# Kernel tuning notes

Measured on AMD Instinct MI355X. Metric: run time of the kernel, lower is better.

Reference implementation:

```python
import jax, jax.numpy as jnp
import numpy as np

H, N, B, L = 256, 64, 4, 2048
LN_EPS = 1e-5


def setup_inputs() -> dict:
    key = jax.random.key(0)
    ks = jax.random.split(key, 10)
    u = jax.random.normal(ks[0], (B, L, H), dtype=jnp.float32)
    # Parameters (HiPPO-eig init replaced by equivalent-range random init; same forward math).
    log_neg_real = jnp.log(jax.random.uniform(ks[1], (N,), minval=0.01, maxval=2.0))
    imag = jax.random.normal(ks[2], (N,)) * 3.0
    B_re = jax.random.normal(ks[3], (H, N)) * 0.01
    B_im = jax.random.normal(ks[4], (H, N)) * 0.01
    C_re = jax.random.normal(ks[5], (H, N)) * 0.01
    C_im = jax.random.normal(ks[6], (H, N)) * 0.01
    D = jax.random.normal(ks[7], (H,)) * 0.01
    log_step = jax.random.uniform(ks[8], (H,), minval=-4.0, maxval=-1.0)
    ln_gamma = jnp.ones((H,), dtype=jnp.float32)
    ln_beta = jnp.zeros((H,), dtype=jnp.float32)
    return {"u": u, "log_neg_real": log_neg_real, "imag": imag,
            "B_re": B_re, "B_im": B_im, "C_re": C_re, "C_im": C_im,
            "D": D, "log_step": log_step, "ln_gamma": ln_gamma, "ln_beta": ln_beta}


def reference(u, log_neg_real, imag, B_re, B_im, C_re, C_im, D, log_step, ln_gamma, ln_beta):
    Bb, Ll, Hh = u.shape
    Lam_re = -jnp.exp(log_neg_real)                      # (N,)
    step = jnp.clip(jnp.exp(log_step), 1e-5, 1.0)        # (H,)
    s_re = step[:, None] * Lam_re[None, :]               # (H,N)
    s_im = step[:, None] * imag[None, :]                 # (H,N)
    Bb_re = B_re * step[:, None]
    Bb_im = B_im * step[:, None]
    CB_re = C_re * Bb_re - C_im * Bb_im                  # (H,N)
    CB_im = C_re * Bb_im + C_im * Bb_re                  # (H,N)
    l_idx = jnp.arange(Ll, dtype=u.dtype)                # (L,)
    ls_re = s_re[:, None, :] * l_idx[None, :, None]      # (H,L,N)
    ls_im = s_im[:, None, :] * l_idx[None, :, None]      # (H,L,N)
    mag = jnp.exp(ls_re)
    K = (jnp.einsum('hn,hln->hl', CB_re, mag * jnp.cos(ls_im))
         - jnp.einsum('hn,hln->hl', CB_im, mag * jnp.sin(ls_im)))  # (H,L)
    # FFT circular conv with zero padding to 2L -> linear conv
    uT = jnp.transpose(u, (0, 2, 1))                     # (B,H,L)
    n = 2 * Ll
    u_f = jnp.fft.rfft(uT, n=n)
    K_f = jnp.fft.rfft(K, n=n)
    y = jnp.fft.irfft(u_f * K_f[None], n=n)[..., :Ll]    # (B,H,L)
    y = y + uT * D[None, :, None]
    y = jnp.transpose(y, (0, 2, 1))                      # (B,L,H)
    y = jax.nn.gelu(y, approximate=False)                # torch nn.GELU default = exact
    # dropout: eval mode (identity)
    mean = jnp.mean(y, axis=-1, keepdims=True)
    var = jnp.var(y, axis=-1, keepdims=True)
    y = (y - mean) / jnp.sqrt(var + LN_EPS) * ln_gamma + ln_beta
    return y
```

## Files before the change

kernel.cpp:

```cpp
#include <hip/hip_runtime.h>
#include <hip/hip_bf16.h>
#include <math.h>

#define Hn 256
#define Nn 64
#define Bn 4
#define Ln 2048
#define NC 32

typedef __attribute__((ext_vector_type(8))) short short8;
typedef __attribute__((ext_vector_type(4))) float f32x4;

#define MFMA16 __builtin_amdgcn_mfma_f32_16x16x32_bf16

#define AF1_STRIDE 8192
#define AF2_STRIDE 12288

__device__ inline short bf16hi(float x) {
    union { __hip_bfloat16 b; unsigned short u; } cv;
    cv.b = __float2bfloat16(x);
    return (short)cv.u;
}
__device__ inline float bf16f(short s) {
    union { __hip_bfloat16 b; unsigned short u; } cv;
    cv.u = (unsigned short)s;
    return __bfloat162float(cv.b);
}

#define CSQ(r, i) { float _nr = (r)*(r) - (i)*(i); (i) = 2.f*(r)*(i); (r) = _nr; }

__global__ __launch_bounds__(256)
void k_pre(const float* __restrict__ u, float* __restrict__ uT,
           const float* __restrict__ lnr, const float* __restrict__ im,
           const float* __restrict__ Bre, const float* __restrict__ Bim,
           const float* __restrict__ Cre, const float* __restrict__ Cim,
           const float* __restrict__ lstep,
           short* __restrict__ AF1, short* __restrict__ AF2,
           float* __restrict__ apar)
{
    __shared__ float sh[2][64][66];
    __shared__ float cbrL[64];
    __shared__ float kb[128];
    int bid = blockIdx.x;
    int tid = threadIdx.x;

    if (bid < 512) {
        int b  = bid >> 7;
        int h0 = ((bid >> 5) & 3) << 6;
        int l0 = (bid & 31) << 6;
        int c4 = tid & 15, rr = tid >> 4;
        #pragma unroll
        for (int i = 0; i < 4; ++i) {
            int r = rr + (i << 4);
            float4 v = *(const float4*)&u[((size_t)b * Ln + l0 + r) * Hn + h0 + (c4 << 2)];
            sh[0][r][(c4 << 2) + 0] = v.x;
            sh[0][r][(c4 << 2) + 1] = v.y;
            sh[0][r][(c4 << 2) + 2] = v.z;
            sh[0][r][(c4 << 2) + 3] = v.w;
        }
        __syncthreads();
        #pragma unroll
        for (int i = 0; i < 4; ++i) {
            int hr = (tid >> 4) + (i << 4);
            int lc = tid & 15;
            float4 v;
            v.x = sh[0][(lc << 2) + 0][hr];
            v.y = sh[0][(lc << 2) + 1][hr];
            v.z = sh[0][(lc << 2) + 2][hr];
            v.w = sh[0][(lc << 2) + 3][hr];
            *(float4*)&uT[((size_t)b * Hn + h0 + hr) * Ln + l0 + (lc << 2)] = v;
        }
        return;
    }

    int h    = bid - 512;
    int lane = tid & 63;
    int wv   = tid >> 6;
    int kq   = lane >> 4;
    int l15  = lane & 15;
    int mrow = (wv << 4) + l15;

    float st  = fminf(fmaxf(expf(lstep[h]), 1e-5f), 1.0f);
    float lam = -expf(lnr[lane]);
    float er  = expf(st * lam);
    float smv = st * im[lane];
    float ar  = er * cosf(smv);
    float ai  = er * sinf(smv);
    float bre = Bre[h * Nn + lane] * st;
    float bim = Bim[h * Nn + lane] * st;
    float crr = Cre[h * Nn + lane];
    float cii = Cim[h * Nn + lane];
    float cbr = crr * bre - cii * bim;
    float cbi = crr * bim + cii * bre;

    float a16r = ar, a16i = ai;
    CSQ(a16r, a16i); CSQ(a16r, a16i); CSQ(a16r, a16i); CSQ(a16r, a16i);
    float a32r = a16r, a32i = a16i; CSQ(a32r, a32i);
    float a48r = a32r * a16r - a32i * a16i;
    float a48i = a32r * a16i + a32i * a16r;
    float a64r = a32r, a64i = a32i; CSQ(a64r, a64i);
    if (tid < 64) {
        apar[(h * Nn + lane) * 2]     = a64r;
        apar[(h * Nn + lane) * 2 + 1] = a64i;
    }

    float pr = 1.f, pi = 0.f;
    if (wv == 1) { pr = a16r; pi = a16i; }
    else if (wv == 2) { pr = a32r; pi = a32i; }
    else if (wv == 3) { pr = a48r; pi = a48i; }
    for (int i = 0; i < 16; ++i) {
        int t = 63 - ((wv << 4) + i);
        sh[0][lane][t] = pr;
        sh[1][lane][t] = pi;
        float nr = pr * ar - pi * ai; pi = pr * ai + pi * ar; pr = nr;
    }
    __syncthreads();

    short* A1h = AF1 + (size_t)h * AF1_STRIDE;
    #pragma unroll
    for (int cm = 0; cm < 2; ++cm)
        #pragma unroll
        for (int kt = 0; kt < 2; ++kt) {
            union { short s[8]; short8 v; } uh;
            #pragma unroll
            for (int j = 0; j < 8; ++j)
                uh.s[j] = bf16hi(sh[cm][mrow][kt * 32 + kq * 8 + j]);
            *(short8*)&A1h[((cm * 4 + wv) * 2 + kt) * 512 + lane * 8] = uh.v;
        }
    __syncthreads();

    if (tid < 64) {
        cbrL[lane] = cbr;
        float Pr = ar, Pi = ai;
        for (int j = 0; j < 64; ++j) {
            sh[0][j][lane] = cbr * Pr - cbi * Pi;
            sh[1][j][lane] = cbr * Pi + cbi * Pr;
            float nr = Pr * ar - Pi * ai; Pi = Pr * ai + Pi * ar; Pr = nr;
        }
    }
    __syncthreads();
    if (tid < 64) kb[tid] = 0.f;
    else if (tid < 128) {
        int t2 = tid - 64;
        float s = 0.f;
        if (t2 == 0) { for (int n2 = 0; n2 < 64; ++n2) s += cbrL[n2]; }
        else         { for (int n2 = 0; n2 < 64; ++n2) s += sh[0][t2 - 1][n2]; }
        kb[tid] = s;
    }
    __syncthreads();

    short* A2h = AF2 + (size_t)h * AF2_STRIDE;
    #pragma unroll
    for (int kt = 0; kt < 6; ++kt) {
        union { short s[8]; short8 v; } uh;
        #pragma unroll
        for (int j = 0; j < 8; ++j) {
            float x;
            if (kt < 2) {
                int kk = kt * 32 + kq * 8 + j;
                x = kb[64 + mrow - kk];
            } else {
                int q2 = kt - 2;
                int nn = (q2 & 1) * 32 + kq * 8 + j;
                x = (q2 >> 1) ? -sh[1][mrow][nn] : sh[0][mrow][nn];
            }
            uh.s[j] = bf16hi(x);
        }
        *(short8*)&A2h[(wv * 6 + kt) * 512 + lane * 8] = uh.v;
    }
}

__global__ __launch_bounds__(256, 4)
void k_scan_chunks(const float* __restrict__ uT, const float* __restrict__ apar,
                   const short* __restrict__ AF1, const short* __restrict__ AF2,
                   const float* __restrict__ D, float* __restrict__ ypre)
{
    __shared__ float P2[64][35][2];
    __shared__ short Sb[2][2][32][72];

    int bh   = blockIdx.x;
    int h    = bh & (Hn - 1);
    int tid  = threadIdx.x;
    int lane = tid & 63;
    int w    = __builtin_amdgcn_readfirstlane(tid >> 6);
    int l15  = lane & 15;
    int kq   = lane >> 4;

    const float* uRow = uT + (size_t)bh * Ln;
    const short* A1h  = AF1 + (size_t)h * AF1_STRIDE;
    const short* A2h  = AF2 + (size_t)h * AF2_STRIDE;

    short8 Uh[2][2], Ul[2][2];
    #pragma unroll
    for (int kt = 0; kt < 2; ++kt)
        #pragma unroll
        for (int ct = 0; ct < 2; ++ct) {
            int c = ct * 16 + l15;
            const float* up = uRow + c * 64 + kt * 32 + kq * 8;
            float4 f0 = *(const float4*)up;
            float4 f1 = *(const float4*)(up + 4);
            float xv[8] = {f0.x, f0.y, f0.z, f0.w, f1.x, f1.y, f1.z, f1.w};
            union { short s[8]; short8 v; } hh, ll;
            #pragma unroll
            for (int j = 0; j < 8; ++j) {
                short hs = bf16hi(xv[j]);
                hh.s[j] = hs;
                ll.s[j] = bf16hi(xv[j] - bf16f(hs));
            }
            Uh[kt][ct] = hh.v;
            Ul[kt][ct] = ll.v;
        }

    f32x4 Pre_acc[2] = {{0.f,0.f,0.f,0.f},{0.f,0.f,0.f,0.f}};
    f32x4 Pim_acc[2] = {{0.f,0.f,0.f,0.f},{0.f,0.f,0.f,0.f}};
    #pragma unroll
    for (int kt = 0; kt < 2; ++kt) {
        short8 a_re = *(const short8*)&A1h[((0 * 4 + w) * 2 + kt) * 512 + lane * 8];
        short8 a_im = *(const short8*)&A1h[((1 * 4 + w) * 2 + kt) * 512 + lane * 8];
        #pragma unroll
        for (int ct = 0; ct < 2; ++ct) {
            Pre_acc[ct] = MFMA16(a_re, Uh[kt][ct], Pre_acc[ct], 0, 0, 0);
            Pre_acc[ct] = MFMA16(a_re, Ul[kt][ct], Pre_acc[ct], 0, 0, 0);
            Pim_acc[ct] = MFMA16(a_im, Uh[kt][ct], Pim_acc[ct], 0, 0, 0);
            Pim_acc[ct] = MFMA16(a_im, Ul[kt][ct], Pim_acc[ct], 0, 0, 0);
        }
    }
    #pragma unroll
    for (int ct = 0; ct < 2; ++ct)
        #pragma unroll
        for (int r = 0; r < 4; ++r) {
            int n = (w << 4) + kq * 4 + r;
            int c = ct * 16 + l15;
            *(float2*)&P2[n][c][0] = make_float2(Pre_acc[ct][r], Pim_acc[ct][r]);
        }
    __syncthreads();

    {
        int n = lane;
        float a64r = apar[(h * Nn + n) * 2];
        float a64i = apar[(h * Nn + n) * 2 + 1];
        float sr = 0.f, si = 0.f;
        for (int c = 0; c < NC; ++c) {
            if ((c >> 3) == w) {
                short hr = bf16hi(sr); short lr = bf16hi(sr - bf16f(hr));
                short hi2 = bf16hi(si); short li = bf16hi(si - bf16f(hi2));
                Sb[0][0][c][n] = hr;  Sb[1][0][c][n] = lr;
                Sb[0][1][c][n] = hi2; Sb[1][1][c][n] = li;
            }
            float2 pv = *(float2*)&P2[n][c][0];
            float nsr = fmaf(a64r, sr, fmaf(-a64i, si, pv.x));
            float nsi = fmaf(a64i, sr, fmaf(a64r, si, pv.y));
            sr = nsr; si = nsi;
        }
    }
    __syncthreads();

    f32x4 Yacc[2] = {{0.f,0.f,0.f,0.f},{0.f,0.f,0.f,0.f}};
    #pragma unroll
    for (int kt = 0; kt < 6; ++kt) {
        short8 a_h = *(const short8*)&A2h[(w * 6 + kt) * 512 + lane * 8];
        #pragma unroll
        for (int ct = 0; ct < 2; ++ct) {
            short8 bhf, blf;
            if (kt < 2) { bhf = Uh[kt][ct]; blf = Ul[kt][ct]; }
            else {
                int q2 = kt - 2, reim = q2 >> 1;
                int nb = (q2 & 1) * 32 + kq * 8;
                int c  = ct * 16 + l15;
                bhf = *(const short8*)&Sb[0][reim][c][nb];
                blf = *(const short8*)&Sb[1][reim][c][nb];
            }
            Yacc[ct] = MFMA16(a_h, bhf, Yacc[ct], 0, 0, 0);
            Yacc[ct] = MFMA16(a_h, blf, Yacc[ct], 0, 0, 0);
        }
    }
    float* Yl = (float*)P2;
    #pragma unroll
    for (int ct = 0; ct < 2; ++ct)
        #pragma unroll
        for (int r = 0; r < 4; ++r) {
            int j = (w << 4) + kq * 4 + r;
            int c = ct * 16 + l15;
            Yl[j * 70 + c] = Yacc[ct][r];
        }
    __syncthreads();

    float Dh = D[h];
    #pragma unroll
    for (int i = 0; i < 8; ++i) {
        int c = (w << 3) + i;
        float y  = Yl[lane * 70 + c];
        float uv = uRow[c * 64 + lane];
        float yv = fmaf(Dh, uv, y);
        float g  = 0.5f * yv * (1.f + erff(yv * 0.70710678118654752f));
        ypre[(size_t)bh * Ln + c * 64 + lane] = g;
    }
}

__global__ __launch_bounds__(256)
void k_ln(const float* __restrict__ ypre, const float* __restrict__ gamma,
          const float* __restrict__ beta, float* __restrict__ out)
{
    __shared__ float tile[32][260];
    int b  = blockIdx.y;
    int l0 = blockIdx.x << 5;
    int t  = threadIdx.x;

    #pragma unroll
    for (int i = 0; i < 8; ++i) {
        int idx = (i << 8) + t;
        int hh  = idx >> 3, lo4 = idx & 7;
        float4 v = *(const float4*)&ypre[((size_t)b * Hn + hh) * Ln + l0 + (lo4 << 2)];
        tile[(lo4 << 2) + 0][hh] = v.x;
        tile[(lo4 << 2) + 1][hh] = v.y;
        tile[(lo4 << 2) + 2][hh] = v.z;
        tile[(lo4 << 2) + 3][hh] = v.w;
    }
    __syncthreads();

    int wv = t >> 6, lane = t & 63;
    float4 g4 = *(const float4*)&gamma[lane << 2];
    float4 b4 = *(const float4*)&beta[lane << 2];
    #pragma unroll
    for (int k = 0; k < 8; ++k) {
        int l = (k << 2) | wv;
        float4 v = *(const float4*)&tile[l][lane << 2];
        float sum = (v.x + v.y) + (v.z + v.w);
        float sq  = fmaf(v.x, v.x, fmaf(v.y, v.y, fmaf(v.z, v.z, v.w * v.w)));
        #pragma unroll
        for (int off = 32; off; off >>= 1) {
            sum += __shfl_xor(sum, off);
            sq  += __shfl_xor(sq, off);
        }
        float mean = sum * (1.f / 256.f);
        float var  = sq * (1.f / 256.f) - mean * mean;
        float rs   = rsqrtf(var + 1e-5f);
        float4 o;
        o.x = (v.x - mean) * rs * g4.x + b4.x;
        o.y = (v.y - mean) * rs * g4.y + b4.y;
        o.z = (v.z - mean) * rs * g4.z + b4.z;
        o.w = (v.w - mean) * rs * g4.w + b4.w;
        *(float4*)&out[((size_t)b * Ln + l0 + l) * Hn + (lane << 2)] = o;
    }
}

extern "C" void kernel_launch(void* const* d_in, const int* in_sizes, int n_in,
                              void* d_out, int out_size, void* d_ws, size_t ws_size,
                              hipStream_t stream)
{
    const float* u     = (const float*)d_in[0];
    const float* lnr   = (const float*)d_in[1];
    const float* im    = (const float*)d_in[2];
    const float* Bre   = (const float*)d_in[3];
    const float* Bim   = (const float*)d_in[4];
    const float* Cre   = (const float*)d_in[5];
    const float* Cim   = (const float*)d_in[6];
    const float* Dp    = (const float*)d_in[7];
    const float* lstep = (const float*)d_in[8];
    const float* gam   = (const float*)d_in[9];
    const float* bet   = (const float*)d_in[10];
    float* out = (float*)d_out;

    float* ws   = (float*)d_ws;
    float* uT   = ws;
    float* apar = uT + (size_t)Bn * Hn * Ln;
    float* ypre = apar + (size_t)Hn * Nn * 2;
    short* AF1  = (short*)(ypre + (size_t)Bn * Hn * Ln);
    short* AF2  = AF1 + (size_t)Hn * AF1_STRIDE;

    k_pre<<<768, 256, 0, stream>>>(u, uT, lnr, im, Bre, Bim, Cre, Cim, lstep, AF1, AF2, apar);
    k_scan_chunks<<<Bn * Hn, 256, 0, stream>>>(uT, apar, AF1, AF2, Dp, ypre);
    k_ln<<<dim3(Ln / 32, Bn), 256, 0, stream>>>(ypre, gam, bet, out);
}
```

Before: 104.8 us.

## Fuse preprocessing into scan kernel, compute operator fragments per block in registers

Merges the transpose/parameter-precompute kernel into the main chunked-scan kernel. Each block now gathers its (b,h) column of u straight into shared memory with strided loads, computes the A1/A2 MFMA operand fragments in registers, and folds D into the kernel diagonal term. This removes one launch and the global round trips for uT, AF1, AF2 and apar. In exchange, the per-h precompute is repeated for every batch element (4x redundant), and the strided global column gather is poorly coalesced.

```diff
diff --git a/kernel.cpp b/kernel.cpp
--- a/kernel.cpp
+++ b/kernel.cpp
@@ -13,9 +13,6 @@
 
 #define MFMA16 __builtin_amdgcn_mfma_f32_16x16x32_bf16
 
-#define AF1_STRIDE 8192
-#define AF2_STRIDE 12288
-
 __device__ inline short bf16hi(float x) {
     union { __hip_bfloat16 b; unsigned short u; } cv;
     cv.b = __float2bfloat16(x);
@@ -29,61 +26,40 @@
 
 #define CSQ(r, i) { float _nr = (r)*(r) - (i)*(i); (i) = 2.f*(r)*(i); (r) = _nr; }
 
-__global__ __launch_bounds__(256)
-void k_pre(const float* __restrict__ u, float* __restrict__ uT,
-           const float* __restrict__ lnr, const float* __restrict__ im,
+__global__ __launch_bounds__(256, 4)
+void k_s4d(const float* __restrict__ u,
+           const float* __restrict__ lnr, const float* __restrict__ imv,
            const float* __restrict__ Bre, const float* __restrict__ Bim,
            const float* __restrict__ Cre, const float* __restrict__ Cim,
-           const float* __restrict__ lstep,
-           short* __restrict__ AF1, short* __restrict__ AF2,
-           float* __restrict__ apar)
+           const float* __restrict__ lstep, const float* __restrict__ Dp,
+           float* __restrict__ ypre)
 {
-    __shared__ float sh[2][64][66];
-    __shared__ float cbrL[64];
-    __shared__ float kb[128];
-    int bid = blockIdx.x;
-    int tid = threadIdx.x;
-
-    if (bid < 512) {
-        int b  = bid >> 7;
-        int h0 = ((bid >> 5) & 3) << 6;
-        int l0 = (bid & 31) << 6;
-        int c4 = tid & 15, rr = tid >> 4;
-        #pragma unroll
-        for (int i = 0; i < 4; ++i) {
-            int r = rr + (i << 4);
-            float4 v = *(const float4*)&u[((size_t)b * Ln + l0 + r) * Hn + h0 + (c4 << 2)];
-            sh[0][r][(c4 << 2) + 0] = v.x;
-            sh[0][r][(c4 << 2) + 1] = v.y;
-            sh[0][r][(c4 << 2) + 2] = v.z;
-            sh[0][r][(c4 << 2) + 3] = v.w;
-        }
-        __syncthreads();
-        #pragma unroll
-        for (int i = 0; i < 4; ++i) {
-            int hr = (tid >> 4) + (i << 4);
-            int lc = tid & 15;
-            float4 v;
-            v.x = sh[0][(lc << 2) + 0][hr];
-            v.y = sh[0][(lc << 2) + 1][hr];
-            v.z = sh[0][(lc << 2) + 2][hr];
-            v.w = sh[0][(lc << 2) + 3][hr];
-            *(float4*)&uT[((size_t)b * Hn + h0 + hr) * Ln + l0 + (lc << 2)] = v;
-        }
-        return;
-    }
-
-    int h    = bid - 512;
-    int lane = tid & 63;
-    int wv   = tid >> 6;
-    int kq   = lane >> 4;
-    int l15  = lane & 15;
-    int mrow = (wv << 4) + l15;
+    __shared__ __align__(16) char smem[36864];
+
+    const int bh   = blockIdx.x;
+    const int b    = bh >> 8;
+    const int h    = bh & (Hn - 1);
+    const int tid  = threadIdx.x;
+    const int lane = tid & 63;
+    const int w    = __builtin_amdgcn_readfirstlane(tid >> 6);
+    const int l15  = lane & 15;
+    const int kq   = lane >> 4;
+    const int mrow = (w << 4) + l15;
+
+    float* us = (float*)smem;
+    {
+        const float* ucol = u + (size_t)b * Ln * Hn + h;
+        #pragma unroll
+        for (int i = 0; i < 8; ++i) {
+            int l = tid + (i << 8);
+            us[(l >> 6) * 68 + (l & 63)] = ucol[(size_t)l * Hn];
+        }
+    }
 
     float st  = fminf(fmaxf(expf(lstep[h]), 1e-5f), 1.0f);
     float lam = -expf(lnr[lane]);
     float er  = expf(st * lam);
-    float smv = st * im[lane];
+    float smv = st * imv[lane];
     float ar  = er * cosf(smv);
     float ai  = er * sinf(smv);
     float bre = Bre[h * Nn + lane] * st;
@@ -92,6 +68,7 @@
     float cii = Cim[h * Nn + lane];
     float cbr = crr * bre - cii * bim;
     float cbi = crr * bim + cii * bre;
+    float Dval = Dp[h];
 
     float a16r = ar, a16i = ai;
     CSQ(a16r, a16i); CSQ(a16r, a16i); CSQ(a16r, a16i); CSQ(a16r, a16i);
@@ -99,96 +76,8 @@
     float a48r = a32r * a16r - a32i * a16i;
     float a48i = a32r * a16i + a32i * a16r;
     float a64r = a32r, a64i = a32i; CSQ(a64r, a64i);
-    if (tid < 64) {
-        apar[(h * Nn + lane) * 2]     = a64r;
-        apar[(h * Nn + lane) * 2 + 1] = a64i;
-    }
-
-    float pr = 1.f, pi = 0.f;
-    if (wv == 1) { pr = a16r; pi = a16i; }
-    else if (wv == 2) { pr = a32r; pi = a32i; }
-    else if (wv == 3) { pr = a48r; pi = a48i; }
-    for (int i = 0; i < 16; ++i) {
-        int t = 63 - ((wv << 4) + i);
-        sh[0][lane][t] = pr;
-        sh[1][lane][t] = pi;
-        float nr = pr * ar - pi * ai; pi = pr * ai + pi * ar; pr = nr;
-    }
-    __syncthreads();
-
-    short* A1h = AF1 + (size_t)h * AF1_STRIDE;
-    #pragma unroll
-    for (int cm = 0; cm < 2; ++cm)
-        #pragma unroll
-        for (int kt = 0; kt < 2; ++kt) {
-            union { short s[8]; short8 v; } uh;
-            #pragma unroll
-            for (int j = 0; j < 8; ++j)
-                uh.s[j] = bf16hi(sh[cm][mrow][kt * 32 + kq * 8 + j]);
-            *(short8*)&A1h[((cm * 4 + wv) * 2 + kt) * 512 + lane * 8] = uh.v;
-        }
-    __syncthreads();
-
-    if (tid < 64) {
-        cbrL[lane] = cbr;
-        float Pr = ar, Pi = ai;
-        for (int j = 0; j < 64; ++j) {
-            sh[0][j][lane] = cbr * Pr - cbi * Pi;
-            sh[1][j][lane] = cbr * Pi + cbi * Pr;
-            float nr = Pr * ar - Pi * ai; Pi = Pr * ai + Pi * ar; Pr = nr;
-        }
-    }
-    __syncthreads();
-    if (tid < 64) kb[tid] = 0.f;
-    else if (tid < 128) {
-        int t2 = tid - 64;
-        float s = 0.f;
-        if (t2 == 0) { for (int n2 = 0; n2 < 64; ++n2) s += cbrL[n2]; }
-        else         { for (int n2 = 0; n2 < 64; ++n2) s += sh[0][t2 - 1][n2]; }
-        kb[tid] = s;
-    }
-    __syncthreads();
-
-    short* A2h = AF2 + (size_t)h * AF2_STRIDE;
-    #pragma unroll
-    for (int kt = 0; kt < 6; ++kt) {
-        union { short s[8]; short8 v; } uh;
-        #pragma unroll
-        for (int j = 0; j < 8; ++j) {
-            float x;
-            if (kt < 2) {
-                int kk = kt * 32 + kq * 8 + j;
-                x = kb[64 + mrow - kk];
-            } else {
-                int q2 = kt - 2;
-                int nn = (q2 & 1) * 32 + kq * 8 + j;
-                x = (q2 >> 1) ? -sh[1][mrow][nn] : sh[0][mrow][nn];
-            }
-            uh.s[j] = bf16hi(x);
-        }
-        *(short8*)&A2h[(wv * 6 + kt) * 512 + lane * 8] = uh.v;
-    }
-}
-
-__global__ __launch_bounds__(256, 4)
-void k_scan_chunks(const float* __restrict__ uT, const float* __restrict__ apar,
-                   const short* __restrict__ AF1, const short* __restrict__ AF2,
-                   const float* __restrict__ D, float* __restrict__ ypre)
-{
-    __shared__ float P2[64][35][2];
-    __shared__ short Sb[2][2][32][72];
-
-    int bh   = blockIdx.x;
-    int h    = bh & (Hn - 1);
-    int tid  = threadIdx.x;
-    int lane = tid & 63;
-    int w    = __builtin_amdgcn_readfirstlane(tid >> 6);
-    int l15  = lane & 15;
-    int kq   = lane >> 4;
-
-    const float* uRow = uT + (size_t)bh * Ln;
-    const short* A1h  = AF1 + (size_t)h * AF1_STRIDE;
-    const short* A2h  = AF2 + (size_t)h * AF2_STRIDE;
+
+    __syncthreads();
 
     short8 Uh[2][2], Ul[2][2];
     #pragma unroll
@@ -196,7 +85,7 @@
         #pragma unroll
         for (int ct = 0; ct < 2; ++ct) {
             int c = ct * 16 + l15;
-            const float* up = uRow + c * 64 + kt * 32 + kq * 8;
+            const float* up = &us[c * 68 + kt * 32 + kq * 8];
             float4 f0 = *(const float4*)up;
             float4 f1 = *(const float4*)(up + 4);
             float xv[8] = {f0.x, f0.y, f0.z, f0.w, f1.x, f1.y, f1.z, f1.w};
@@ -211,20 +100,99 @@
             Ul[kt][ct] = ll.v;
         }
 
+    __syncthreads();
+
+    float (*shA)[64][66] = (float (*)[64][66])smem;
+    float* cbrL = (float*)(smem + 33792);
+    float* kb   = (float*)(smem + 34048);
+    {
+        float pr = 1.f, pi = 0.f;
+        if (w == 1)      { pr = a16r; pi = a16i; }
+        else if (w == 2) { pr = a32r; pi = a32i; }
+        else if (w == 3) { pr = a48r; pi = a48i; }
+        for (int i = 0; i < 16; ++i) {
+            int t = 63 - ((w << 4) + i);
+            shA[0][lane][t] = pr;
+            shA[1][lane][t] = pi;
+            float nr = pr * ar - pi * ai; pi = pr * ai + pi * ar; pr = nr;
+        }
+    }
+    __syncthreads();
+
+    short8 A1f[2][2];
+    #pragma unroll
+    for (int cm = 0; cm < 2; ++cm)
+        #pragma unroll
+        for (int kt = 0; kt < 2; ++kt) {
+            union { short s[8]; short8 v; } uh;
+            #pragma unroll
+            for (int j = 0; j < 8; ++j)
+                uh.s[j] = bf16hi(shA[cm][mrow][kt * 32 + kq * 8 + j]);
+            A1f[cm][kt] = uh.v;
+        }
+    __syncthreads();
+
+    {
+        float Pr, Pi;
+        if (w == 0)      { Pr = ar; Pi = ai; }
+        else if (w == 1) { Pr = a16r * ar - a16i * ai; Pi = a16r * ai + a16i * ar; }
+        else if (w == 2) { Pr = a32r * ar - a32i * ai; Pi = a32r * ai + a32i * ar; }
+        else             { Pr = a48r * ar - a48i * ai; Pi = a48r * ai + a48i * ar; }
+        if (tid < 64) cbrL[lane] = cbr;
+        for (int i = 0; i < 16; ++i) {
+            int j = (w << 4) + i;
+            shA[0][j][lane] = cbr * Pr - cbi * Pi;
+            shA[1][j][lane] = cbr * Pi + cbi * Pr;
+            float nr = Pr * ar - Pi * ai; Pi = Pr * ai + Pi * ar; Pr = nr;
+        }
+    }
+    __syncthreads();
+
+    if (tid < 64) kb[tid] = 0.f;
+    else if (tid < 128) {
+        int t2 = tid - 64;
+        float s = 0.f;
+        if (t2 == 0) { for (int n2 = 0; n2 < 64; ++n2) s += cbrL[n2]; s += Dval; }
+        else         { for (int n2 = 0; n2 < 64; ++n2) s += shA[0][t2 - 1][n2]; }
+        kb[tid] = s;
+    }
+    __syncthreads();
+
+    short8 A2f[6];
+    #pragma unroll
+    for (int kt = 0; kt < 6; ++kt) {
+        union { short s[8]; short8 v; } uh;
+        #pragma unroll
+        for (int j = 0; j < 8; ++j) {
+            float x;
+            if (kt < 2) {
+                int kk = kt * 32 + kq * 8 + j;
+                x = kb[64 + mrow - kk];
+            } else {
+                int q2 = kt - 2;
+                int nn = (q2 & 1) * 32 + kq * 8 + j;
+                x = (q2 >> 1) ? -shA[1][mrow][nn] : shA[0][mrow][nn];
+            }
+            uh.s[j] = bf16hi(x);
+        }
+        A2f[kt] = uh.v;
+    }
+    __syncthreads();
+
     f32x4 Pre_acc[2] = {{0.f,0.f,0.f,0.f},{0.f,0.f,0.f,0.f}};
     f32x4 Pim_acc[2] = {{0.f,0.f,0.f,0.f},{0.f,0.f,0.f,0.f}};
     #pragma unroll
     for (int kt = 0; kt < 2; ++kt) {
-        short8 a_re = *(const short8*)&A1h[((0 * 4 + w) * 2 + kt) * 512 + lane * 8];
-        short8 a_im = *(const short8*)&A1h[((1 * 4 + w) * 2 + kt) * 512 + lane * 8];
         #pragma unroll
         for (int ct = 0; ct < 2; ++ct) {
-            Pre_acc[ct] = MFMA16(a_re, Uh[kt][ct], Pre_acc[ct], 0, 0, 0);
-            Pre_acc[ct] = MFMA16(a_re, Ul[kt][ct], Pre_acc[ct], 0, 0, 0);
-            Pim_acc[ct] = MFMA16(a_im, Uh[kt][ct], Pim_acc[ct], 0, 0, 0);
-            Pim_acc[ct] = MFMA16(a_im, Ul[kt][ct], Pim_acc[ct], 0, 0, 0);
-        }
-    }
+            Pre_acc[ct] = MFMA16(A1f[0][kt], Uh[kt][ct], Pre_acc[ct], 0, 0, 0);
+            Pre_acc[ct] = MFMA16(A1f[0][kt], Ul[kt][ct], Pre_acc[ct], 0, 0, 0);
+            Pim_acc[ct] = MFMA16(A1f[1][kt], Uh[kt][ct], Pim_acc[ct], 0, 0, 0);
+            Pim_acc[ct] = MFMA16(A1f[1][kt], Ul[kt][ct], Pim_acc[ct], 0, 0, 0);
+        }
+    }
+    float (*P2)[35][2]     = (float (*)[35][2])smem;
+    short (*Sb)[2][32][72] = (short (*)[2][32][72])(smem + 17920);
     #pragma unroll
     for (int ct = 0; ct < 2; ++ct)
         #pragma unroll
@@ -237,8 +205,6 @@
 
     {
         int n = lane;
-        float a64r = apar[(h * Nn + n) * 2];
-        float a64i = apar[(h * Nn + n) * 2 + 1];
         float sr = 0.f, si = 0.f;
         for (int c = 0; c < NC; ++c) {
             if ((c >> 3) == w) {
@@ -258,7 +224,6 @@
     f32x4 Yacc[2] = {{0.f,0.f,0.f,0.f},{0.f,0.f,0.f,0.f}};
     #pragma unroll
     for (int kt = 0; kt < 6; ++kt) {
-        short8 a_h = *(const short8*)&A2h[(w * 6 + kt) * 512 + lane * 8];
         #pragma unroll
         for (int ct = 0; ct < 2; ++ct) {
             short8 bhf, blf;
@@ -270,11 +235,11 @@
                 bhf = *(const short8*)&Sb[0][reim][c][nb];
                 blf = *(const short8*)&Sb[1][reim][c][nb];
             }
-            Yacc[ct] = MFMA16(a_h, bhf, Yacc[ct], 0, 0, 0);
-            Yacc[ct] = MFMA16(a_h, blf, Yacc[ct], 0, 0, 0);
-        }
-    }
-    float* Yl = (float*)P2;
+            Yacc[ct] = MFMA16(A2f[kt], bhf, Yacc[ct], 0, 0, 0);
+            Yacc[ct] = MFMA16(A2f[kt], blf, Yacc[ct], 0, 0, 0);
+        }
+    }
+    float* Yl = (float*)smem;
     #pragma unroll
     for (int ct = 0; ct < 2; ++ct)
         #pragma unroll
@@ -285,14 +250,11 @@
         }
     __syncthreads();
 
-    float Dh = D[h];
     #pragma unroll
     for (int i = 0; i < 8; ++i) {
         int c = (w << 3) + i;
-        float y  = Yl[lane * 70 + c];
-        float uv = uRow[c * 64 + lane];
-        float yv = fmaf(Dh, uv, y);
-        float g  = 0.5f * yv * (1.f + erff(yv * 0.70710678118654752f));
+        float y = Yl[lane * 70 + c];
+        float g = 0.5f * y * (1.f + erff(y * 0.70710678118654752f));
         ypre[(size_t)bh * Ln + c * 64 + lane] = g;
     }
 }
@@ -361,14 +323,8 @@
     const float* bet   = (const float*)d_in[10];
     float* out = (float*)d_out;
 
-    float* ws   = (float*)d_ws;
-    float* uT   = ws;
-    float* apar = uT + (size_t)Bn * Hn * Ln;
-    float* ypre = apar + (size_t)Hn * Nn * 2;
-    short* AF1  = (short*)(ypre + (size_t)Bn * Hn * Ln);
-    short* AF2  = AF1 + (size_t)Hn * AF1_STRIDE;
-
-    k_pre<<<768, 256, 0, stream>>>(u, uT, lnr, im, Bre, Bim, Cre, Cim, lstep, AF1, AF2, apar);
-    k_scan_chunks<<<Bn * Hn, 256, 0, stream>>>(uT, apar, AF1, AF2, Dp, ypre);
+    float* ypre = (float*)d_ws;
+
+    k_s4d<<<Bn * Hn, 256, 0, stream>>>(u, lnr, im, Bre, Bim, Cre, Cim, lstep, Dp, ypre);
     k_ln<<<dim3(Ln / 32, Bn), 256, 0, stream>>>(ypre, gam, bet, out);
 }
```

Result: no change. 105.6 us (+0.8%).
